# Optimization experiments

Hardware: AMD Instinct MI355X
Metric: run time of the kernel (lower is better)

Reference implementation:

```python
import jax, jax.numpy as jnp
import numpy as np

KERNEL_SIZE = 5
SIGMA_SPACE = 1.0
SIGMA_COLOR = 0.1
PAD = KERNEL_SIZE // 2


def make_spatial_kernel(kernel_size, sigma_space):
    r = kernel_size // 2
    coords = jnp.arange(-r, r + 1, dtype=jnp.float32)
    xx, yy = jnp.meshgrid(coords, coords, indexing='ij')
    return jnp.exp(-(xx ** 2 + yy ** 2) / (2.0 * sigma_space ** 2))  # [K, K]


def setup_inputs() -> dict:
    key = jax.random.key(0)
    x = jax.random.uniform(key, (4, 3, 512, 512), dtype=jnp.float32)
    spatial_kernel = make_spatial_kernel(KERNEL_SIZE, SIGMA_SPACE)
    sigma_color = jnp.float32(SIGMA_COLOR)
    return {"x": x, "spatial_kernel": spatial_kernel, "sigma_color": sigma_color}


def reference(x, spatial_kernel, sigma_color):
    # x: [B, C, H, W]; spatial_kernel: [K, K] (fixed buffer, computed at init)
    B, C, H, W = x.shape
    K = KERNEL_SIZE
    padded = jnp.pad(x, ((0, 0), (0, 0), (PAD, PAD), (PAD, PAD)), mode='reflect')
    # Gather KxK windows as a trailing tap axis: [B, C, H, W, K*K]
    patches = jnp.stack(
        [padded[:, :, i:i + H, j:j + W] for i in range(K) for j in range(K)],
        axis=-1,
    )
    sk = spatial_kernel.reshape(-1)  # [K*K]
    color_diff = patches - x[..., None]
    color_weight = jnp.exp(-(color_diff ** 2) / (2.0 * sigma_color ** 2))
    weight = sk * color_weight  # [B, C, H, W, K*K]
    weight = weight / (jnp.sum(weight, axis=-1, keepdims=True) + 1e-8)
    return jnp.sum(weight * patches, axis=-1)  # [B, C, H, W]
```

## Files before the change

### kernel.cpp

```cpp
#include <hip/hip_runtime.h>

typedef float v2f __attribute__((ext_vector_type(2)));

constexpr int H = 512, W = 512;
constexpr int K = 5, PADR = 2;
constexpr int ROWS = 4;
constexpr int SROWS = ROWS + 4;

__device__ __forceinline__ float rfl(float v) {
    union { float f; int i; } u; u.f = v;
    u.i = __builtin_amdgcn_readfirstlane(u.i);
    return u.f;
}

constexpr int idx6(int d2) {
    return d2 == 0 ? 0 : d2 == 1 ? 1 : d2 == 2 ? 2 : d2 == 4 ? 3 : d2 == 5 ? 4 : 5;
}

__global__ __launch_bounds__(256, 4) void bilateral_kernel(
    const float* __restrict__ x,
    const float* __restrict__ sk,
    const float* __restrict__ sigma_color,
    float* __restrict__ out)
{
    __shared__ float lds[SROWS][W];

    int t = threadIdx.x;
    int wave = t >> 6;
    int l = t & 63;

    float lw[6];
    lw[0] = rfl(__builtin_amdgcn_logf(sk[12]));
    lw[1] = rfl(__builtin_amdgcn_logf(sk[7]));
    lw[2] = rfl(__builtin_amdgcn_logf(sk[6]));
    lw[3] = rfl(__builtin_amdgcn_logf(sk[2]));
    lw[4] = rfl(__builtin_amdgcn_logf(sk[1]));
    lw[5] = rfl(__builtin_amdgcn_logf(sk[0]));

    float s = sigma_color[0];
    float c2 = -1.4426950408889634f / (2.0f * s * s);
    v2f c2v = { c2, c2 };

    int plane = blockIdx.x >> 7;
    int r0 = (blockIdx.x & 127) * ROWS;
    const float* xp = x + (size_t)plane * (H * W);

#pragma unroll
    for (int kk = 0; kk < 2; ++kk) {
        int k = wave + 4 * kk;
        int gr = r0 - 2 + k;
        gr = (gr < 0) ? -gr : gr;
        gr = (gr >= H) ? (2 * H - 2 - gr) : gr;
        const float* src = xp + (gr << 9) + (l << 3);
        float4 v0 = *(const float4*)(src);
        float4 v1 = *(const float4*)(src + 4);
        *(float4*)(&lds[k][l << 3])     = v0;
        *(float4*)(&lds[k][(l << 3) + 4]) = v1;
    }
    __syncthreads();

    int rr = wave;
    int w0 = l << 3;

    bool lane0 = (l == 0);
    bool laneN = (l == 63);
    int wL = lane0 ? 0       : (w0 - 4);
    int wR = laneN ? (w0 + 4) : (w0 + 8);

    v2f cc[4], ws[4], acc[4];
#pragma unroll
    for (int q = 0; q < 4; ++q) { ws[q] = (v2f){0.f, 0.f}; acc[q] = (v2f){0.f, 0.f}; }

    constexpr int order[K] = {2, 0, 1, 3, 4};
#pragma unroll
    for (int oi = 0; oi < K; ++oi) {
        const int i = order[oi];
        const float* rp = &lds[rr + i][0];

        float4 a  = *(const float4*)(rp + wL);
        float4 m0 = *(const float4*)(rp + w0);
        float4 m1 = *(const float4*)(rp + w0 + 4);
        float4 b  = *(const float4*)(rp + wR);

        float win[12];
        win[0]  = lane0 ? m0.z : a.z;
        win[1]  = lane0 ? m0.y : a.w;
        win[2]  = m0.x; win[3] = m0.y; win[4] = m0.z; win[5] = m0.w;
        win[6]  = m1.x; win[7] = m1.y; win[8] = m1.z; win[9] = m1.w;
        win[10] = laneN ? m1.z : b.x;
        win[11] = laneN ? m1.y : b.y;

        if (oi == 0) {
#pragma unroll
            for (int q = 0; q < 4; ++q) {
                cc[q][0] = win[2 * q + 2];
                cc[q][1] = win[2 * q + 3];
            }
        }

#pragma unroll
        for (int j = 0; j < K; ++j) {
            const float lwv = lw[idx6((i - 2) * (i - 2) + (j - 2) * (j - 2))];
            v2f lsp = { lwv, lwv };
#pragma unroll
            for (int q = 0; q < 4; ++q) {
                v2f v = { win[2 * q + j], win[2 * q + j + 1] };
                v2f d = v - cc[q];
                v2f arg = __builtin_elementwise_fma(d * c2v, d, lsp);
                v2f wq;
                wq[0] = __builtin_amdgcn_exp2f(arg[0]);
                wq[1] = __builtin_amdgcn_exp2f(arg[1]);
                ws[q] += wq;
                acc[q] = __builtin_elementwise_fma(wq, v, acc[q]);
            }
        }
    }

    float* op = out + (size_t)plane * (H * W) + ((r0 + rr) << 9) + w0;
    float4 o0, o1;
    o0.x = acc[0][0] * __builtin_amdgcn_rcpf(ws[0][0] + 1e-8f);
    o0.y = acc[0][1] * __builtin_amdgcn_rcpf(ws[0][1] + 1e-8f);
    o0.z = acc[1][0] * __builtin_amdgcn_rcpf(ws[1][0] + 1e-8f);
    o0.w = acc[1][1] * __builtin_amdgcn_rcpf(ws[1][1] + 1e-8f);
    o1.x = acc[2][0] * __builtin_amdgcn_rcpf(ws[2][0] + 1e-8f);
    o1.y = acc[2][1] * __builtin_amdgcn_rcpf(ws[2][1] + 1e-8f);
    o1.z = acc[3][0] * __builtin_amdgcn_rcpf(ws[3][0] + 1e-8f);
    o1.w = acc[3][1] * __builtin_amdgcn_rcpf(ws[3][1] + 1e-8f);
    *(float4*)(op)     = o0;
    *(float4*)(op + 4) = o1;
}

extern "C" void kernel_launch(void* const* d_in, const int* in_sizes, int n_in,
                              void* d_out, int out_size, void* d_ws, size_t ws_size,
                              hipStream_t stream) {
    const float* x  = (const float*)d_in[0];
    const float* sk = (const float*)d_in[1];
    const float* sc = (const float*)d_in[2];
    float* out = (float*)d_out;

    const int total = in_sizes[0];
    const int blocks = total / (256 * 8);
    bilateral_kernel<<<blocks, 256, 0, stream>>>(x, sk, sc, out);
}
```

Baseline: 78.48 us.

## Halve per-thread work to 4 pixels, 2-row tiles, skip center-tap exp

Changes the tiling so each block covers 2 output rows with 4 pixels per thread instead of 4 rows with 8 pixels. That doubles the grid size and cuts register use, at the cost of more halo rows reloaded into LDS per output row (6 loaded for 2 computed versus 8 for 4). The packed v2f math becomes scalar. The center tap's weight is now the constant spatial value (color difference is zero), so its exp is skipped.

```diff
diff --git a/kernel.cpp b/kernel.cpp
--- a/kernel.cpp
+++ b/kernel.cpp
@@ -1,11 +1,9 @@
 #include <hip/hip_runtime.h>
-
-typedef float v2f __attribute__((ext_vector_type(2)));
 
 constexpr int H = 512, W = 512;
 constexpr int K = 5, PADR = 2;
-constexpr int ROWS = 4;
-constexpr int SROWS = ROWS + 4;
+constexpr int TR = 2;
+constexpr int SR = TR + 4;
 
 __device__ __forceinline__ float rfl(float v) {
     union { float f; int i; } u; u.f = v;
@@ -23,10 +21,10 @@
     const float* __restrict__ sigma_color,
     float* __restrict__ out)
 {
-    __shared__ float lds[SROWS][W];
+    __shared__ float lds[SR][W];
 
     int t = threadIdx.x;
-    int wave = t >> 6;
+    int wv = t >> 6;
     int l = t & 63;
 
     float lw[6];
@@ -36,40 +34,37 @@
     lw[3] = rfl(__builtin_amdgcn_logf(sk[2]));
     lw[4] = rfl(__builtin_amdgcn_logf(sk[1]));
     lw[5] = rfl(__builtin_amdgcn_logf(sk[0]));
+    float sk12 = rfl(sk[12]);
 
     float s = sigma_color[0];
     float c2 = -1.4426950408889634f / (2.0f * s * s);
-    v2f c2v = { c2, c2 };
 
-    int plane = blockIdx.x >> 7;
-    int r0 = (blockIdx.x & 127) * ROWS;
+    int plane = blockIdx.x >> 8;
+    int r0 = (blockIdx.x & 255) << 1;
     const float* xp = x + (size_t)plane * (H * W);
 
 #pragma unroll
-    for (int kk = 0; kk < 2; ++kk) {
-        int k = wave + 4 * kk;
+    for (int su = 0; su < 3; ++su) {
+        int u = wv + (su << 2);
+        int k = u >> 1, hh = u & 1;
         int gr = r0 - 2 + k;
         gr = (gr < 0) ? -gr : gr;
         gr = (gr >= H) ? (2 * H - 2 - gr) : gr;
-        const float* src = xp + (gr << 9) + (l << 3);
-        float4 v0 = *(const float4*)(src);
-        float4 v1 = *(const float4*)(src + 4);
-        *(float4*)(&lds[k][l << 3])     = v0;
-        *(float4*)(&lds[k][(l << 3) + 4]) = v1;
+        int col = (hh << 8) + (l << 2);
+        float4 v = *(const float4*)(xp + (gr << 9) + col);
+        *(float4*)(&lds[k][col]) = v;
     }
     __syncthreads();
 
-    int rr = wave;
-    int w0 = l << 3;
+    int rr = wv >> 1;
+    int c  = ((wv & 1) << 6) + l;
+    bool le = (c == 0), re = (c == 127);
+    int cm1 = le ? 0   : c - 1;
+    int cp1 = re ? 127 : c + 1;
 
-    bool lane0 = (l == 0);
-    bool laneN = (l == 63);
-    int wL = lane0 ? 0       : (w0 - 4);
-    int wR = laneN ? (w0 + 4) : (w0 + 8);
-
-    v2f cc[4], ws[4], acc[4];
+    float cc[4], wsum[4], acc[4];
 #pragma unroll
-    for (int q = 0; q < 4; ++q) { ws[q] = (v2f){0.f, 0.f}; acc[q] = (v2f){0.f, 0.f}; }
+    for (int p = 0; p < 4; ++p) { wsum[p] = 0.f; acc[p] = 0.f; }
 
     constexpr int order[K] = {2, 0, 1, 3, 4};
 #pragma unroll
@@ -77,57 +72,52 @@
         const int i = order[oi];
         const float* rp = &lds[rr + i][0];
 
-        float4 a  = *(const float4*)(rp + wL);
-        float4 m0 = *(const float4*)(rp + w0);
-        float4 m1 = *(const float4*)(rp + w0 + 4);
-        float4 b  = *(const float4*)(rp + wR);
+        float4 a = *(const float4*)(rp + (cm1 << 2));
+        float4 m = *(const float4*)(rp + (c   << 2));
+        float4 b = *(const float4*)(rp + (cp1 << 2));
 
-        float win[12];
-        win[0]  = lane0 ? m0.z : a.z;
-        win[1]  = lane0 ? m0.y : a.w;
-        win[2]  = m0.x; win[3] = m0.y; win[4] = m0.z; win[5] = m0.w;
-        win[6]  = m1.x; win[7] = m1.y; win[8] = m1.z; win[9] = m1.w;
-        win[10] = laneN ? m1.z : b.x;
-        win[11] = laneN ? m1.y : b.y;
+        float win[8];
+        win[0] = le ? m.z : a.z;
+        win[1] = le ? m.y : a.w;
+        win[2] = m.x; win[3] = m.y; win[4] = m.z; win[5] = m.w;
+        win[6] = re ? m.z : b.x;
+        win[7] = re ? m.y : b.y;
 
         if (oi == 0) {
 #pragma unroll
-            for (int q = 0; q < 4; ++q) {
-                cc[q][0] = win[2 * q + 2];
-                cc[q][1] = win[2 * q + 3];
-            }
+            for (int p = 0; p < 4; ++p) cc[p] = win[p + 2];
         }
 
 #pragma unroll
         for (int j = 0; j < K; ++j) {
-            const float lwv = lw[idx6((i - 2) * (i - 2) + (j - 2) * (j - 2))];
-            v2f lsp = { lwv, lwv };
+            if (i == 2 && j == 2) {
 #pragma unroll
-            for (int q = 0; q < 4; ++q) {
-                v2f v = { win[2 * q + j], win[2 * q + j + 1] };
-                v2f d = v - cc[q];
-                v2f arg = __builtin_elementwise_fma(d * c2v, d, lsp);
-                v2f wq;
-                wq[0] = __builtin_amdgcn_exp2f(arg[0]);
-                wq[1] = __builtin_amdgcn_exp2f(arg[1]);
-                ws[q] += wq;
-                acc[q] = __builtin_elementwise_fma(wq, v, acc[q]);
+                for (int p = 0; p < 4; ++p) {
+                    wsum[p] += sk12;
+                    acc[p] = __builtin_fmaf(sk12, cc[p], acc[p]);
+                }
+            } else {
+                const float lwv = lw[idx6((i - 2) * (i - 2) + (j - 2) * (j - 2))];
+#pragma unroll
+                for (int p = 0; p < 4; ++p) {
+                    float v = win[p + j];
+                    float d = v - cc[p];
+                    float arg = __builtin_fmaf(d * c2, d, lwv);
+                    float wq = __builtin_amdgcn_exp2f(arg);
+                    wsum[p] += wq;
+                    acc[p] = __builtin_fmaf(wq, v, acc[p]);
+                }
             }
         }
     }
 
-    float* op = out + (size_t)plane * (H * W) + ((r0 + rr) << 9) + w0;
-    float4 o0, o1;
-    o0.x = acc[0][0] * __builtin_amdgcn_rcpf(ws[0][0] + 1e-8f);
-    o0.y = acc[0][1] * __builtin_amdgcn_rcpf(ws[0][1] + 1e-8f);
-    o0.z = acc[1][0] * __builtin_amdgcn_rcpf(ws[1][0] + 1e-8f);
-    o0.w = acc[1][1] * __builtin_amdgcn_rcpf(ws[1][1] + 1e-8f);
-    o1.x = acc[2][0] * __builtin_amdgcn_rcpf(ws[2][0] + 1e-8f);
-    o1.y = acc[2][1] * __builtin_amdgcn_rcpf(ws[2][1] + 1e-8f);
-    o1.z = acc[3][0] * __builtin_amdgcn_rcpf(ws[3][0] + 1e-8f);
-    o1.w = acc[3][1] * __builtin_amdgcn_rcpf(ws[3][1] + 1e-8f);
-    *(float4*)(op)     = o0;
-    *(float4*)(op + 4) = o1;
+    float* op = out + (size_t)plane * (H * W) + ((size_t)(r0 + rr) << 9) + (c << 2);
+    float4 o;
+    o.x = acc[0] * __builtin_amdgcn_rcpf(wsum[0] + 1e-8f);
+    o.y = acc[1] * __builtin_amdgcn_rcpf(wsum[1] + 1e-8f);
+    o.z = acc[2] * __builtin_amdgcn_rcpf(wsum[2] + 1e-8f);
+    o.w = acc[3] * __builtin_amdgcn_rcpf(wsum[3] + 1e-8f);
+    *(float4*)op = o;
 }
 
 extern "C" void kernel_launch(void* const* d_in, const int* in_sizes, int n_in,
@@ -139,6 +129,6 @@
     float* out = (float*)d_out;
 
     const int total = in_sizes[0];
-    const int blocks = total / (256 * 8);
+    const int blocks = total / (256 * 4);
     bilateral_kernel<<<blocks, 256, 0, stream>>>(x, sk, sc, out);
 }
```

Measured after the change: 82.17 us. 1.05x slower.
